# Kernel tuning notes

Measured on AMD Instinct MI355X. Metric: run time of the kernel, lower is better.

The kernel has to match this reference:

```python
import jax, jax.numpy as jnp
import numpy as np

D = 4096  # in_features == rotation_size (power of 2 -> K == 1, no extra hadamard_K matmul)


def matmul_hadU(x):
    """Normalized Walsh-Hadamard transform along the last axis, matching the
    torch recursive-butterfly matmul_hadU (K == 1 branch)."""
    n = x.shape[-1]
    shape = x.shape
    v = x.reshape(-1, n, 1)  # (B*, m, c) with m*c == n
    while v.shape[1] > 1:
        b_, m, c = v.shape
        v = v.reshape(b_, m // 2, 2, c)
        a, b = v[:, :, 0, :], v[:, :, 1, :]
        # view(b_, m//2, 2*c): [a+b | a-b] along the channel axis
        v = jnp.concatenate([a + b, a - b], axis=-1)
    return v.reshape(shape) / jnp.sqrt(jnp.asarray(n, x.dtype))


def setup_inputs() -> dict:
    key = jax.random.key(0)
    k_x, k_w, k_b = jax.random.split(key, 3)
    x = jax.random.normal(k_x, (4, 2048, D), dtype=jnp.float32)
    W = jax.random.normal(k_w, (D, D), dtype=jnp.float32) * 0.02  # nn.Linear weight [out, in]
    b = jax.random.normal(k_b, (D,), dtype=jnp.float32) * 0.02
    return {"x": x, "W": W, "b": b}


def reference(x, W, b):
    x_rot = matmul_hadU(x)                 # [B, S, D]
    return jnp.einsum('bsd,od->bso', x_rot, W) + b
```

## Files before the change

### kernel.cpp

```cpp
#include <hip/hip_runtime.h>
#include <hip/hip_bf16.h>


#define D_DIM 4096
#define M_ROWS 8192

typedef float f32x4 __attribute__((ext_vector_type(4)));
typedef __bf16 bf16x8 __attribute__((ext_vector_type(8)));

__device__ __forceinline__ unsigned short f2bf(float f) {
  unsigned int u = __float_as_uint(f);
  return (unsigned short)((u + 0x7fffu + ((u >> 16) & 1u)) >> 16);
}

__device__ __forceinline__ void async16(const void* g, void* l) {
  __builtin_amdgcn_global_load_lds(
      (const __attribute__((address_space(1))) unsigned int*)g,
      (__attribute__((address_space(3))) unsigned int*)l, 16, 0, 0);
}

#define WHT_AS 280
#define WHT_BS 17

__global__ __launch_bounds__(256) void wht_cast_rows(
    const float* __restrict__ X, unsigned short* __restrict__ Y) {
  __shared__ float s[16 * WHT_AS];
  const int row = blockIdx.x;
  const float* xr = X + (size_t)row * D_DIM;
  const int t = threadIdx.x;
  float v[16];

#pragma unroll
  for (int a = 0; a < 16; ++a) v[a] = xr[a * 256 + t];
#pragma unroll
  for (int h = 1; h < 16; h <<= 1) {
#pragma unroll
    for (int i = 0; i < 16; ++i) {
      if ((i & h) == 0) {
        float p = v[i], q = v[i + h];
        v[i] = p + q;
        v[i + h] = p - q;
      }
    }
  }
  {
    const int base = (t >> 4) * WHT_BS + (t & 15);
#pragma unroll
    for (int a = 0; a < 16; ++a) s[a * WHT_AS + base] = v[a];
  }
  __syncthreads();

  {
    const int base = (t >> 4) * WHT_AS + (t & 15);
#pragma unroll
    for (int b = 0; b < 16; ++b) v[b] = s[base + b * WHT_BS];
#pragma unroll
    for (int h = 1; h < 16; h <<= 1) {
#pragma unroll
      for (int i = 0; i < 16; ++i) {
        if ((i & h) == 0) {
          float p = v[i], q = v[i + h];
          v[i] = p + q;
          v[i + h] = p - q;
        }
      }
    }
#pragma unroll
    for (int b = 0; b < 16; ++b) s[base + b * WHT_BS] = v[b];
  }
  __syncthreads();

  {
    const int base = (t >> 4) * WHT_AS + (t & 15) * WHT_BS;
#pragma unroll
    for (int c = 0; c < 16; ++c) v[c] = s[base + c];
#pragma unroll
    for (int h = 1; h < 16; h <<= 1) {
#pragma unroll
      for (int i = 0; i < 16; ++i) {
        if ((i & h) == 0) {
          float p = v[i], q = v[i + h];
          v[i] = p + q;
          v[i + h] = p - q;
        }
      }
    }
    union {
      unsigned short us[16];
      uint4 q4[2];
    } pk;
#pragma unroll
    for (int c = 0; c < 16; ++c) pk.us[c] = f2bf(v[c] * 0.015625f);
    uint4* dst =
        (uint4*)(Y + (size_t)row * D_DIM + (t >> 4) * 256 + (t & 15) * 16);
    dst[0] = pk.q4[0];
    dst[1] = pk.q4[1];
  }
}

__global__ __launch_bounds__(256) void cast_w(const float* __restrict__ W,
                                              unsigned short* __restrict__ Wb) {
  const size_t i = ((size_t)blockIdx.x * 256 + threadIdx.x) * 8;
  const float4* p = (const float4*)(W + i);
  float4 f0 = p[0], f1 = p[1];
  union {
    unsigned short us[8];
    uint4 q;
  } pk;
  pk.us[0] = f2bf(f0.x);
  pk.us[1] = f2bf(f0.y);
  pk.us[2] = f2bf(f0.z);
  pk.us[3] = f2bf(f0.w);
  pk.us[4] = f2bf(f1.x);
  pk.us[5] = f2bf(f1.y);
  pk.us[6] = f2bf(f1.z);
  pk.us[7] = f2bf(f1.w);
  *(uint4*)(Wb + i) = pk.q;
}

#define GNT 64

__global__ __launch_bounds__(512, 2) void gemm256_bias(
    const unsigned short* __restrict__ A,
    const unsigned short* __restrict__ B,
    const float* __restrict__ bias, float* __restrict__ C) {
  constexpr int K = 4096, N = 4096;
  __shared__ unsigned short sm[65536];

  const int tid = threadIdx.x;
  const int l = tid & 63;
  const int w = tid >> 6;
  const int wm = w >> 2;
  const int wn = w & 3;
  const int row16 = l & 15;
  const int kgrp = l >> 4;

  const int orig = blockIdx.x;
  const int wgid = (orig & 7) * 64 + (orig >> 3);
  const int bn = wgid & 15;
  const int bm = wgid >> 4;
  const int m0 = bm * 256, n0 = bn * 256;

  const int srcRow = (w >> 1) * 16 + (l >> 2);
  const int srcCol = (w & 1) * 32 + ((((l & 3) << 4) ^ ((l >> 5) << 5)) >> 1);
  const unsigned short* aS = A + (size_t)(m0 + srcRow) * K + srcCol;
  const unsigned short* bS = B + (size_t)(n0 + srcRow) * K + srcCol;
  const int dstBase = tid * 8;

#define STG_A(b, h, kt)                                                       \
  do {                                                                        \
    async16(aS + (size_t)((h)*128) * K + (kt)*64,                             \
            &sm[(b)*32768 + (h)*8192 + dstBase]);                             \
    async16(aS + (size_t)((h)*128 + 64) * K + (kt)*64,                        \
            &sm[(b)*32768 + (h)*8192 + 4096 + dstBase]);                      \
  } while (0)
#define STG_B(b, h, kt)                                                       \
  do {                                                                        \
    async16(bS + (size_t)((h)*128) * K + (kt)*64,                             \
            &sm[(b)*32768 + 16384 + (h)*8192 + dstBase]);                     \
    async16(bS + (size_t)((h)*128 + 64) * K + (kt)*64,                        \
            &sm[(b)*32768 + 16384 + (h)*8192 + 4096 + dstBase]);              \
  } while (0)

  const int laneRd = row16 * 32 + ((kgrp << 3) ^ ((row16 >> 3) << 4));

  f32x4 acc[8][4];
#pragma unroll
  for (int i = 0; i < 8; ++i)
#pragma unroll
    for (int j = 0; j < 4; ++j) acc[i][j] = (f32x4){0.f, 0.f, 0.f, 0.f};

  STG_A(0, 0, 0);
  STG_A(0, 1, 0);
  STG_B(0, 0, 0);
  STG_B(0, 1, 0);
  STG_A(1, 0, 1);
  STG_A(1, 1, 1);
  STG_B(1, 0, 1);
  asm volatile("s_waitcnt vmcnt(6)" ::: "memory");
  __builtin_amdgcn_s_barrier();

#define MFMA_G(MB, NB)                                                       \
  _Pragma("unroll") for (int ks = 0; ks < 2; ++ks)                           \
      _Pragma("unroll") for (int mf = 0; mf < 4; ++mf)                       \
          _Pragma("unroll") for (int nf = 0; nf < 2; ++nf) acc[MB + mf]      \
              [NB + nf] = __builtin_amdgcn_mfma_f32_16x16x32_bf16(           \
                  af[MB + mf][ks], bfm[NB + nf][ks], acc[MB + mf][NB + nf],  \
                  0, 0, 0);

  int cur = 0;
  for (int T = 0; T < GNT; ++T) {
    const int base = cur * 32768;
    const unsigned short* pA = &sm[base + wm * 8192 + laneRd];
    const unsigned short* pB =
        &sm[base + 16384 + (wn >> 1) * 8192 + (wn & 1) * 4096 + laneRd];
    bf16x8 af[8][2], bfm[4][2];

#pragma unroll
    for (int mf = 0; mf < 4; ++mf) {
      af[mf][0] = *(const bf16x8*)&pA[mf * 1024];
      af[mf][1] = *(const bf16x8*)&pA[mf * 1024 + 512];
    }
#pragma unroll
    for (int nf = 0; nf < 2; ++nf) {
      bfm[nf][0] = *(const bf16x8*)&pB[nf * 1024];
      bfm[nf][1] = *(const bf16x8*)&pB[nf * 1024 + 512];
    }
    if (T + 1 < GNT) STG_B(cur ^ 1, 1, T + 1);
    asm volatile("s_waitcnt lgkmcnt(8)" ::: "memory");
    __builtin_amdgcn_s_barrier();
    asm volatile("s_waitcnt lgkmcnt(0)" ::: "memory");
    __builtin_amdgcn_s_setprio(1);
    MFMA_G(0, 0);
    __builtin_amdgcn_s_setprio(0);
    __builtin_amdgcn_s_barrier();

#pragma unroll
    for (int mf = 4; mf < 8; ++mf) {
      af[mf][0] = *(const bf16x8*)&pA[mf * 1024];
      af[mf][1] = *(const bf16x8*)&pA[mf * 1024 + 512];
    }
    asm volatile("s_waitcnt lgkmcnt(4)" ::: "memory");
    __builtin_amdgcn_s_barrier();
    asm volatile("s_waitcnt lgkmcnt(0)" ::: "memory");
    __builtin_amdgcn_s_setprio(1);
    MFMA_G(4, 0);
    __builtin_amdgcn_s_setprio(0);
    __builtin_amdgcn_s_barrier();

#pragma unroll
    for (int nf = 2; nf < 4; ++nf) {
      bfm[nf][0] = *(const bf16x8*)&pB[nf * 1024];
      bfm[nf][1] = *(const bf16x8*)&pB[nf * 1024 + 512];
    }
    if (T + 2 < GNT) STG_A(cur, 0, T + 2);
    __builtin_amdgcn_s_barrier();
    asm volatile("s_waitcnt lgkmcnt(0)" ::: "memory");
    __builtin_amdgcn_s_setprio(1);
    MFMA_G(0, 2);
    __builtin_amdgcn_s_setprio(0);
    __builtin_amdgcn_s_barrier();

    if (T + 2 < GNT) {
      STG_A(cur, 1, T + 2);
      STG_B(cur, 0, T + 2);
    }
    __builtin_amdgcn_s_barrier();
    __builtin_amdgcn_s_setprio(1);
    MFMA_G(4, 2);
    __builtin_amdgcn_s_setprio(0);
    if (T < GNT - 2)
      asm volatile("s_waitcnt vmcnt(6)" ::: "memory");
    else
      asm volatile("s_waitcnt vmcnt(0)" ::: "memory");
    __builtin_amdgcn_s_barrier();
    cur ^= 1;
  }

  const int mb = m0 + wm * 128 + kgrp * 4;
  const int nb = n0 + wn * 64 + row16;
  float bv[4];
#pragma unroll
  for (int nf = 0; nf < 4; ++nf) bv[nf] = bias[nb + nf * 16];
#pragma unroll
  for (int mf = 0; mf < 8; ++mf)
#pragma unroll
    for (int nf = 0; nf < 4; ++nf)
#pragma unroll
      for (int r = 0; r < 4; ++r)
        C[(size_t)(mb + mf * 16 + r) * N + nb + nf * 16] =
            acc[mf][nf][r] + bv[nf];
}

extern "C" void kernel_launch(void* const* d_in, const int* in_sizes, int n_in,
                              void* d_out, int out_size, void* d_ws,
                              size_t ws_size, hipStream_t stream) {
  const float* x = (const float*)d_in[0];
  const float* W = (const float*)d_in[1];
  const float* b = (const float*)d_in[2];
  float* out = (float*)d_out;

  unsigned short* Xr = (unsigned short*)d_ws;
  unsigned short* Wb = Xr + (size_t)M_ROWS * D_DIM;

  wht_cast_rows<<<M_ROWS, 256, 0, stream>>>(x, Xr);
  cast_w<<<(D_DIM * (size_t)D_DIM / 8) / 256, 256, 0, stream>>>(W, Wb);
  gemm256_bias<<<512, 512, 0, stream>>>(Xr, Wb, b, out);
}
```

Before: 495.0 us.

## Prefetch next tile's first LDS fragments during last MFMA group

Restructures the GEMM main loop into a software pipeline. The first A/B fragment reads for the next K tile are hoisted into the previous iteration, issued before the final MFMA quadrant so LDS reads overlap with matrix work. The global-to-LDS staging order is also reshuffled, and the vmcnt wait moves earlier to guard the new cross-iteration read. Explicit lgkmcnt waits are removed in favour of compiler-inserted ones. This adds register pressure and relies on correct barrier placement to avoid reading LDS that is still being written.

```diff
diff --git a/kernel.cpp b/kernel.cpp
--- a/kernel.cpp
+++ b/kernel.cpp
@@ -188,71 +188,90 @@
                   af[MB + mf][ks], bfm[NB + nf][ks], acc[MB + mf][NB + nf],  \
                   0, 0, 0);
 
+  bf16x8 af[8][2], bfm[4][2];
+
+  {
+    const unsigned short* pA = &sm[wm * 8192 + laneRd];
+    const unsigned short* pB =
+        &sm[16384 + (wn >> 1) * 8192 + (wn & 1) * 4096 + laneRd];
+#pragma unroll
+    for (int mf = 0; mf < 4; ++mf) {
+      af[mf][0] = *(const bf16x8*)&pA[mf * 1024];
+      af[mf][1] = *(const bf16x8*)&pA[mf * 1024 + 512];
+    }
+#pragma unroll
+    for (int nf = 0; nf < 2; ++nf) {
+      bfm[nf][0] = *(const bf16x8*)&pB[nf * 1024];
+      bfm[nf][1] = *(const bf16x8*)&pB[nf * 1024 + 512];
+    }
+  }
+
   int cur = 0;
   for (int T = 0; T < GNT; ++T) {
     const int base = cur * 32768;
     const unsigned short* pA = &sm[base + wm * 8192 + laneRd];
     const unsigned short* pB =
         &sm[base + 16384 + (wn >> 1) * 8192 + (wn & 1) * 4096 + laneRd];
-    bf16x8 af[8][2], bfm[4][2];
-
-#pragma unroll
-    for (int mf = 0; mf < 4; ++mf) {
+
+    if (T + 1 < GNT) STG_B(cur ^ 1, 1, T + 1);
+#pragma unroll
+    for (int mf = 4; mf < 8; ++mf) {
       af[mf][0] = *(const bf16x8*)&pA[mf * 1024];
       af[mf][1] = *(const bf16x8*)&pA[mf * 1024 + 512];
     }
-#pragma unroll
-    for (int nf = 0; nf < 2; ++nf) {
-      bfm[nf][0] = *(const bf16x8*)&pB[nf * 1024];
-      bfm[nf][1] = *(const bf16x8*)&pB[nf * 1024 + 512];
-    }
-    if (T + 1 < GNT) STG_B(cur ^ 1, 1, T + 1);
-    asm volatile("s_waitcnt lgkmcnt(8)" ::: "memory");
-    __builtin_amdgcn_s_barrier();
-    asm volatile("s_waitcnt lgkmcnt(0)" ::: "memory");
+    __builtin_amdgcn_s_barrier();
     __builtin_amdgcn_s_setprio(1);
     MFMA_G(0, 0);
     __builtin_amdgcn_s_setprio(0);
     __builtin_amdgcn_s_barrier();
 
 #pragma unroll
-    for (int mf = 4; mf < 8; ++mf) {
-      af[mf][0] = *(const bf16x8*)&pA[mf * 1024];
-      af[mf][1] = *(const bf16x8*)&pA[mf * 1024 + 512];
-    }
-    asm volatile("s_waitcnt lgkmcnt(4)" ::: "memory");
-    __builtin_amdgcn_s_barrier();
-    asm volatile("s_waitcnt lgkmcnt(0)" ::: "memory");
+    for (int nf = 2; nf < 4; ++nf) {
+      bfm[nf][0] = *(const bf16x8*)&pB[nf * 1024];
+      bfm[nf][1] = *(const bf16x8*)&pB[nf * 1024 + 512];
+    }
+    __builtin_amdgcn_s_barrier();
     __builtin_amdgcn_s_setprio(1);
     MFMA_G(4, 0);
     __builtin_amdgcn_s_setprio(0);
     __builtin_amdgcn_s_barrier();
 
-#pragma unroll
-    for (int nf = 2; nf < 4; ++nf) {
-      bfm[nf][0] = *(const bf16x8*)&pB[nf * 1024];
-      bfm[nf][1] = *(const bf16x8*)&pB[nf * 1024 + 512];
-    }
-    if (T + 2 < GNT) STG_A(cur, 0, T + 2);
-    __builtin_amdgcn_s_barrier();
-    asm volatile("s_waitcnt lgkmcnt(0)" ::: "memory");
+    if (T + 2 < GNT) {
+      STG_A(cur, 0, T + 2);
+      STG_A(cur, 1, T + 2);
+    }
+    __builtin_amdgcn_s_barrier();
     __builtin_amdgcn_s_setprio(1);
     MFMA_G(0, 2);
     __builtin_amdgcn_s_setprio(0);
     __builtin_amdgcn_s_barrier();
 
-    if (T + 2 < GNT) {
-      STG_A(cur, 1, T + 2);
-      STG_B(cur, 0, T + 2);
-    }
-    __builtin_amdgcn_s_barrier();
+    if (T + 2 < GNT) STG_B(cur, 0, T + 2);
+    if (T < GNT - 2)
+      asm volatile("s_waitcnt vmcnt(6)" ::: "memory");
+    else if (T == GNT - 2)
+      asm volatile("s_waitcnt vmcnt(0)" ::: "memory");
+    __builtin_amdgcn_s_barrier();
+    if (T + 1 < GNT) {
+      const int base2 = (cur ^ 1) * 32768;
+      const unsigned short* pA2 = &sm[base2 + wm * 8192 + laneRd];
+      const unsigned short* pB2 =
+          &sm[base2 + 16384 + (wn >> 1) * 8192 + (wn & 1) * 4096 + laneRd];
+#pragma unroll
+      for (int mf = 0; mf < 4; ++mf) {
+        af[mf][0] = *(const bf16x8*)&pA2[mf * 1024];
+        af[mf][1] = *(const bf16x8*)&pA2[mf * 1024 + 512];
+      }
+#pragma unroll
+      for (int nf = 0; nf < 2; ++nf) {
+        bfm[nf][0] = *(const bf16x8*)&pB2[nf * 1024];
+        bfm[nf][1] = *(const bf16x8*)&pB2[nf * 1024 + 512];
+      }
+    }
+    __builtin_amdgcn_sched_barrier(0);
     __builtin_amdgcn_s_setprio(1);
     MFMA_G(4, 2);
     __builtin_amdgcn_s_setprio(0);
-    if (T < GNT - 2)
-      asm volatile("s_waitcnt vmcnt(6)" ::: "memory");
-    else
-      asm volatile("s_waitcnt vmcnt(0)" ::: "memory");
     __builtin_amdgcn_s_barrier();
     cur ^= 1;
   }
```

After: 489.7 us. About the same (-1.1%).
